# Performance work log

Hardware: AMD Instinct MI355X
Metric: run time of the kernel (lower is better)

The kernel has to match this reference:

```python
import jax, jax.numpy as jnp
import numpy as np

NUM_NODE_TYPES = 4
NUM_EDGE_TYPES = 12
OUT_SHAPE = (3, 3)


def setup_inputs() -> dict:
    key = jax.random.key(0)
    k1, k2, k3, k4, k5 = jax.random.split(key, 5)
    N, E, C = 100000, 1600000, 64
    in_dim = C * 2 + NUM_NODE_TYPES * 2 + NUM_EDGE_TYPES  # 148
    out_dim = int(np.prod(OUT_SHAPE))  # 9
    return {
        "x": jax.random.normal(k1, (N, C), dtype=jnp.float32),
        "edge_index": jax.random.randint(k2, (2, E), 0, N, dtype=jnp.int64),
        "edge_types": jax.random.randint(k3, (E,), 0, NUM_EDGE_TYPES, dtype=jnp.int64),
        "node_types": jax.random.randint(k4, (N,), 0, NUM_NODE_TYPES, dtype=jnp.int64),
        "W": jax.random.normal(k5, (out_dim, in_dim), dtype=jnp.float32) * 0.08,
    }


def reference(x, edge_index, edge_types, node_types, W):
    src, dst = edge_index[0], edge_index[1]
    x_src = x[src]                      # [E, C]
    x_dst = x[dst]                      # [E, C]
    nt_oh = jax.nn.one_hot(node_types, NUM_NODE_TYPES, dtype=x.dtype)  # [N, 4]
    src_type = nt_oh[src]               # [E, 4]
    dst_type = nt_oh[dst]               # [E, 4]
    edge_type = jax.nn.one_hot(edge_types, NUM_EDGE_TYPES, dtype=x.dtype)  # [E, 12]
    x_cat = jnp.concatenate([x_src, x_dst, src_type, dst_type, edge_type], axis=1)  # [E, 148]
    maps = x_cat @ W.T                  # [E, 9], bias-free linear
    maps = jnp.tanh(maps)
    return maps.reshape(-1, OUT_SHAPE[0], OUT_SHAPE[1])
```

## Files before the change

kernel.cpp:

```cpp
#include <hip/hip_runtime.h>
#include <math.h>

#define C 64
#define IN_DIM 148
#define ODIM 9

typedef _Float16 half_t;
typedef float f4 __attribute__((ext_vector_type(4)));
typedef _Float16 h2 __attribute__((ext_vector_type(2)));
typedef unsigned int u32;
typedef u32 u4 __attribute__((ext_vector_type(4)));

__device__ __forceinline__ float tanh_fast(float x) {
    float e = __expf(2.0f * x);
    return 1.0f - 2.0f / (e + 1.0f);
}

__device__ __forceinline__ void decode9(u4 w, int u[ODIM]) {
    u[0] = w.x & 0xFFF;
    u[1] = (w.x >> 12) & 0xFFF;
    u[2] = __builtin_amdgcn_alignbit(w.y, w.x, 24) & 0xFFF;
    u[3] = (w.y >> 4) & 0xFFF;
    u[4] = (w.y >> 16) & 0xFFF;
    u[5] = __builtin_amdgcn_alignbit(w.z, w.y, 28) & 0xFFF;
    u[6] = (w.z >> 8) & 0xFFF;
    u[7] = (w.z >> 20) & 0xFFF;
    u[8] = w.w & 0xFFF;
}

__device__ __forceinline__ void gather2_sc0(const u4* a, const u4* b,
                                            u4& ra, u4& rb) {
    asm volatile(
        "global_load_dwordx4 %0, %2, off sc0\n\t"
        "global_load_dwordx4 %1, %3, off sc0\n\t"
        "s_waitcnt vmcnt(0)"
        : "=&v"(ra), "=&v"(rb)
        : "v"(a), "v"(b));
}

__global__ __launch_bounds__(256) void node_proj_kernel(
    const float* __restrict__ x, const int* __restrict__ node_types,
    const float* __restrict__ W, u4* __restrict__ sp, u4* __restrict__ dp,
    int N)
{
    __shared__ _Float16 Wh[2 * ODIM][C];
    __shared__ float ntab[2][ODIM][4];

    for (int i = threadIdx.x; i < 2 * ODIM * C; i += 256) {
        int r = i >> 6, c = i & 63;
        int o = (r < ODIM) ? r : r - ODIM;
        int col = (r < ODIM) ? c : (C + c);
        Wh[r][c] = (_Float16)W[o * IN_DIM + col];
    }
    for (int i = threadIdx.x; i < 2 * ODIM * 4; i += 256) {
        int t = i & 3;
        int o = (i >> 2) % ODIM;
        int sd = (i >> 2) / ODIM;
        ntab[sd][o][t] = W[o * IN_DIM + 128 + sd * 4 + t];
    }
    __syncthreads();

    int tid = blockIdx.x * 256 + threadIdx.x;
    int n = tid >> 1;
    int h = tid & 1;
    if (n >= N) return;

    const f4* xr = (const f4*)(x + (size_t)n * C);
    h2 xh[32];
#pragma unroll
    for (int q = 0; q < 16; ++q) {
        f4 v = xr[q];
        xh[2 * q]     = h2{(_Float16)v.x, (_Float16)v.y};
        xh[2 * q + 1] = h2{(_Float16)v.z, (_Float16)v.w};
    }

    float acc[ODIM];
#pragma unroll
    for (int o = 0; o < ODIM; ++o) acc[o] = 0.0f;

#pragma unroll
    for (int g = 0; g < 8; ++g) {
#pragma unroll
        for (int o = 0; o < ODIM; ++o) {
            const h2* wp = (const h2*)&Wh[h * ODIM + o][g * 8];
            acc[o] = __builtin_amdgcn_fdot2(xh[4 * g + 0], wp[0], acc[o], false);
            acc[o] = __builtin_amdgcn_fdot2(xh[4 * g + 1], wp[1], acc[o], false);
            acc[o] = __builtin_amdgcn_fdot2(xh[4 * g + 2], wp[2], acc[o], false);
            acc[o] = __builtin_amdgcn_fdot2(xh[4 * g + 3], wp[3], acc[o], false);
        }
    }

    int t = node_types[n];
    u32 u[ODIM];
#pragma unroll
    for (int o = 0; o < ODIM; ++o) {
        float v = acc[o] + ntab[h][o][t];
        int q = (int)rintf(fmaf(v, 256.0f, 2048.0f));
        q = q < 0 ? 0 : (q > 4095 ? 4095 : q);
        u[o] = (u32)q;
    }
    u4 w;
    w.x = u[0] | (u[1] << 12) | (u[2] << 24);
    w.y = (u[2] >> 8) | (u[3] << 4) | (u[4] << 16) | (u[5] << 28);
    w.z = (u[5] >> 4) | (u[6] << 8) | (u[7] << 20);
    w.w = u[8];

    (h ? dp : sp)[n] = w;
}

__global__ __launch_bounds__(256) void edge_kernel(
    const int* __restrict__ ei, const int* __restrict__ etypes,
    const u4* __restrict__ sp, const u4* __restrict__ dp,
    const float* __restrict__ W, float* __restrict__ out,
    int E)
{
    __shared__ float etab2[12][ODIM];
    __shared__ alignas(16) float sm[256 * ODIM];

    for (int i = threadIdx.x; i < 12 * ODIM; i += 256) {
        int t = i / ODIM, o = i - t * ODIM;
        etab2[t][o] = W[o * IN_DIM + 136 + t] - 16.0f;
    }
    __syncthreads();

    int base = blockIdx.x * 256;
    int e = base + threadIdx.x;
    int cnt = E - base; if (cnt > 256) cnt = 256;

    if (threadIdx.x < cnt) {
        int s  = __builtin_nontemporal_load(ei + e);
        int d  = __builtin_nontemporal_load(ei + (size_t)E + e);
        int et = __builtin_nontemporal_load(etypes + e);

        u4 sw, dw;
        gather2_sc0(sp + s, dp + d, sw, dw);

        int us[ODIM], ud[ODIM];
        decode9(sw, us);
        decode9(dw, ud);

        const float* eb = &etab2[et][0];
#pragma unroll
        for (int o = 0; o < ODIM; ++o) {
            float v = fmaf((float)(us[o] + ud[o]), 1.0f / 256.0f, eb[o]);
            sm[threadIdx.x * ODIM + o] = tanh_fast(v);
        }
    }
    __syncthreads();

    float* ob = out + (size_t)base * ODIM;
    if (cnt == 256) {
        const f4* smv = (const f4*)sm;
        f4* obv = (f4*)ob;
#pragma unroll
        for (int j = threadIdx.x; j < 256 * ODIM / 4; j += 256)
            __builtin_nontemporal_store(smv[j], obv + j);
    } else {
        int tot = cnt * ODIM;
        for (int j = threadIdx.x; j < tot; j += 256)
            __builtin_nontemporal_store(sm[j], ob + j);
    }
}

extern "C" void kernel_launch(void* const* d_in, const int* in_sizes, int n_in,
                              void* d_out, int out_size, void* d_ws, size_t ws_size,
                              hipStream_t stream) {
    const float* x      = (const float*)d_in[0];
    const int*   ei     = (const int*)d_in[1];
    const int*   etypes = (const int*)d_in[2];
    const int*   ntypes = (const int*)d_in[3];
    const float* W      = (const float*)d_in[4];
    float* out = (float*)d_out;

    int N = in_sizes[0] / C;
    int E = in_sizes[2];

    u4* sp = (u4*)d_ws;
    u4* dp = sp + N;

    int nthreads = N * 2;
    int nblocks  = (nthreads + 255) / 256;
    node_proj_kernel<<<nblocks, 256, 0, stream>>>(x, ntypes, W, sp, dp, N);

    int eblocks = (E + 255) / 256;
    edge_kernel<<<eblocks, 256, 0, stream>>>(ei, etypes, sp, dp, W, out, E);
}
```

Measured before the change: 42.57 us.

## Split node projection across four lanes with shuffled x halves and reduction

The node projection kernel now uses four threads per node instead of two. Each thread loads a distinct 16-float chunk of the node row with sc0 inline asm, exchanges chunks with its neighbour lane via shuffles, and computes a half-length dot product over a 32-column slice. Partial sums are combined with a cross-lane shuffle and only one lane per pair packs and writes the result. This removes the duplicate x reads, where both threads previously loaded the full row, and raises parallelism, at the cost of extra shuffles and twice as many threads.

```diff
diff --git a/kernel.cpp b/kernel.cpp
--- a/kernel.cpp
+++ b/kernel.cpp
@@ -38,6 +38,18 @@
         : "v"(a), "v"(b));
 }
 
+__device__ __forceinline__ void load4x16_sc0(const float* p, u4& a0, u4& a1,
+                                             u4& a2, u4& a3) {
+    asm volatile(
+        "global_load_dwordx4 %0, %4, off sc0\n\t"
+        "global_load_dwordx4 %1, %4, off offset:16 sc0\n\t"
+        "global_load_dwordx4 %2, %4, off offset:32 sc0\n\t"
+        "global_load_dwordx4 %3, %4, off offset:48 sc0\n\t"
+        "s_waitcnt vmcnt(0)"
+        : "=&v"(a0), "=&v"(a1), "=&v"(a2), "=&v"(a3)
+        : "v"(p));
+}
+
 __global__ __launch_bounds__(256) void node_proj_kernel(
     const float* __restrict__ x, const int* __restrict__ node_types,
     const float* __restrict__ W, u4* __restrict__ sp, u4* __restrict__ dp,
@@ -61,17 +73,32 @@
     __syncthreads();
 
     int tid = blockIdx.x * 256 + threadIdx.x;
-    int n = tid >> 1;
-    int h = tid & 1;
+    int n  = tid >> 2;
+    int q  = tid & 3;
+    int h  = q & 1;
+    int ch = q >> 1;
     if (n >= N) return;
 
-    const f4* xr = (const f4*)(x + (size_t)n * C);
-    h2 xh[32];
-#pragma unroll
-    for (int q = 0; q < 16; ++q) {
-        f4 v = xr[q];
-        xh[2 * q]     = h2{(_Float16)v.x, (_Float16)v.y};
-        xh[2 * q + 1] = h2{(_Float16)v.z, (_Float16)v.w};
+    const float* xp = x + (size_t)n * C + q * 16;
+    u4 xc[4];
+    load4x16_sc0(xp, xc[0], xc[1], xc[2], xc[3]);
+
+    u4 xn[4];
+#pragma unroll
+    for (int i = 0; i < 4; ++i)
+#pragma unroll
+        for (int j = 0; j < 4; ++j)
+            xn[i][j] = (u32)__shfl_xor((int)xc[i][j], 1);
+
+    h2 xh[16];
+#pragma unroll
+    for (int i = 0; i < 4; ++i) {
+        u4 a = (q & 1) ? xn[i] : xc[i];
+        u4 b = (q & 1) ? xc[i] : xn[i];
+        xh[2 * i]     = h2{(_Float16)__uint_as_float(a.x), (_Float16)__uint_as_float(a.y)};
+        xh[2 * i + 1] = h2{(_Float16)__uint_as_float(a.z), (_Float16)__uint_as_float(a.w)};
+        xh[8 + 2 * i]     = h2{(_Float16)__uint_as_float(b.x), (_Float16)__uint_as_float(b.y)};
+        xh[8 + 2 * i + 1] = h2{(_Float16)__uint_as_float(b.z), (_Float16)__uint_as_float(b.w)};
     }
 
     float acc[ODIM];
@@ -79,10 +106,10 @@
     for (int o = 0; o < ODIM; ++o) acc[o] = 0.0f;
 
 #pragma unroll
-    for (int g = 0; g < 8; ++g) {
+    for (int g = 0; g < 4; ++g) {
 #pragma unroll
         for (int o = 0; o < ODIM; ++o) {
-            const h2* wp = (const h2*)&Wh[h * ODIM + o][g * 8];
+            const h2* wp = (const h2*)&Wh[h * ODIM + o][ch * 32 + g * 8];
             acc[o] = __builtin_amdgcn_fdot2(xh[4 * g + 0], wp[0], acc[o], false);
             acc[o] = __builtin_amdgcn_fdot2(xh[4 * g + 1], wp[1], acc[o], false);
             acc[o] = __builtin_amdgcn_fdot2(xh[4 * g + 2], wp[2], acc[o], false);
@@ -90,22 +117,27 @@
         }
     }
 
-    int t = node_types[n];
-    u32 u[ODIM];
-#pragma unroll
-    for (int o = 0; o < ODIM; ++o) {
-        float v = acc[o] + ntab[h][o][t];
-        int q = (int)rintf(fmaf(v, 256.0f, 2048.0f));
-        q = q < 0 ? 0 : (q > 4095 ? 4095 : q);
-        u[o] = (u32)q;
-    }
-    u4 w;
-    w.x = u[0] | (u[1] << 12) | (u[2] << 24);
-    w.y = (u[2] >> 8) | (u[3] << 4) | (u[4] << 16) | (u[5] << 28);
-    w.z = (u[5] >> 4) | (u[6] << 8) | (u[7] << 20);
-    w.w = u[8];
-
-    (h ? dp : sp)[n] = w;
+#pragma unroll
+    for (int o = 0; o < ODIM; ++o)
+        acc[o] += __shfl_xor(acc[o], 2);
+
+    if (ch == 0) {
+        int t = node_types[n];
+        u32 u[ODIM];
+#pragma unroll
+        for (int o = 0; o < ODIM; ++o) {
+            float v = acc[o] + ntab[h][o][t];
+            int qi = (int)rintf(fmaf(v, 256.0f, 2048.0f));
+            qi = qi < 0 ? 0 : (qi > 4095 ? 4095 : qi);
+            u[o] = (u32)qi;
+        }
+        u4 w;
+        w.x = u[0] | (u[1] << 12) | (u[2] << 24);
+        w.y = (u[2] >> 8) | (u[3] << 4) | (u[4] << 16) | (u[5] << 28);
+        w.z = (u[5] >> 4) | (u[6] << 8) | (u[7] << 20);
+        w.w = u[8];
+        (h ? dp : sp)[n] = w;
+    }
 }
 
 __global__ __launch_bounds__(256) void edge_kernel(
@@ -178,7 +210,7 @@
     u4* sp = (u4*)d_ws;
     u4* dp = sp + N;
 
-    int nthreads = N * 2;
+    int nthreads = N * 4;
     int nblocks  = (nthreads + 255) / 256;
     node_proj_kernel<<<nblocks, 256, 0, stream>>>(x, ntypes, W, sp, dp, N);
 
```

Result: no change. 42.42 us (-0.3%).
